# Kernel optimization log

Measured on AMD Instinct MI355X. Metric: run time of the kernel, lower is better.

## Reference

```python
import jax, jax.numpy as jnp
import numpy as np
from math import sqrt

D_LLM = 768
N_HEADS = 8
D_KEYS = 128


def setup_inputs() -> dict:
    key = jax.random.key(0)
    ks = jax.random.split(key, 9)
    B, T, N, S = 8, 96, 16, 1000
    dkh = D_KEYS * N_HEADS
    inp = {
        "time_series": jax.random.normal(ks[0], (B, T, N), dtype=jnp.float32),
        "source_embedding": jax.random.normal(ks[1], (S, D_LLM), dtype=jnp.float32),
        "value_embedding": jax.random.normal(ks[2], (S, D_LLM), dtype=jnp.float32),
        # key_projection: Linear(d_llm, d_keys*n_heads)
        "Wk": jax.random.normal(ks[3], (D_LLM, dkh), dtype=jnp.float32) / np.float32(sqrt(D_LLM)),
        "bk": jnp.zeros((dkh,), dtype=jnp.float32),
        # value_projection: Linear(d_llm, d_keys*n_heads)
        "Wv": jax.random.normal(ks[4], (D_LLM, dkh), dtype=jnp.float32) / np.float32(sqrt(D_LLM)),
        "bv": jnp.zeros((dkh,), dtype=jnp.float32),
        # out_projection: Linear(d_keys*n_heads, d_llm)
        "Wo": jax.random.normal(ks[5], (dkh, D_LLM), dtype=jnp.float32) / np.float32(sqrt(dkh)),
        "bo": jnp.zeros((D_LLM,), dtype=jnp.float32),
    }
    return inp


def reference(time_series, source_embedding, value_embedding, Wk, bk, Wv, bv, Wo, bo):
    B, T, N = time_series.shape
    S = source_embedding.shape[0]
    H, dk = N_HEADS, D_KEYS

    # (B,T,N) -> (B*N, T); Q repeats each scalar across d_keys*n_heads then nan->0
    ts = jnp.transpose(time_series, (0, 2, 1)).reshape(B * N, T)
    ts = jnp.where(jnp.isnan(ts), jnp.float32(0.0), ts)
    Q = jnp.broadcast_to(ts[:, :, None, None], (B * N, T, H, dk))  # bthe

    K = (source_embedding @ Wk + bk).reshape(S, H, dk)  # she
    V = (value_embedding @ Wv + bv).reshape(S, H, dk)   # she

    scale = jnp.float32(1.0 / sqrt(dk))
    scores = jnp.einsum('bthe,she->bhts', Q, K)          # [B*N, H, T, S]
    A = jax.nn.softmax(scale * scores, axis=-1)          # dropout = identity (eval)
    out = jnp.einsum('bhts,she->bthe', A, V).reshape(B * N, T, H * dk)
    return out @ Wo + bo                                 # [B*N, T, d_llm]
```

## Files before the change

kernel.cpp:

```cpp
#include <hip/hip_runtime.h>
#include <hip/hip_bf16.h>
#include <math.h>

#define D_LLM 768
#define DKH   1024
#define NH    8
#define DK    128
#define S_LEN 1000
#define S_PAD 1024
#define M_ROWS 12288
#define T_LEN 96
#define N_VARS 16

static constexpr float SCALE_EXP2 = (float)(0.08838834764831845 * 1.4426950408889634);

typedef __attribute__((ext_vector_type(8))) _Float16 half8;
typedef __attribute__((ext_vector_type(2))) _Float16 half2v;
typedef __attribute__((ext_vector_type(4))) float f32x4;

__device__ __forceinline__ half2v pkrtz(float a, float b) {
    return __builtin_bit_cast(half2v, __builtin_amdgcn_cvt_pkrtz(a, b));
}

__device__ __forceinline__ void gload_lds16(const void* g, void* l) {
    __builtin_amdgcn_global_load_lds(
        (const __attribute__((address_space(1))) unsigned int*)g,
        (__attribute__((address_space(3))) unsigned int*)l, 16, 0, 0);
}

__global__ __launch_bounds__(256) void prep_kernel(const float* __restrict__ vemb,
                                                   const float* __restrict__ Wv,
                                                   const float* __restrict__ Wo,
                                                   const float* __restrict__ Wk,
                                                   const float* __restrict__ bk,
                                                   _Float16* __restrict__ Ab16,
                                                   _Float16* __restrict__ Wvt,
                                                   _Float16* __restrict__ Wot,
                                                   float* __restrict__ Wksum,
                                                   float* __restrict__ bksum) {
    __shared__ float tl[32][33];
    int blk = blockIdx.x, tid = threadIdx.x;
    if (blk < 768) {
        int i4 = (blk * 256 + tid) * 4;
        float4 v = make_float4(0.f, 0.f, 0.f, 0.f);
        if (i4 < S_LEN * D_LLM) v = *(const float4*)(vemb + i4);
        short4 o;
        o.x = __builtin_bit_cast(short, (_Float16)v.x);
        o.y = __builtin_bit_cast(short, (_Float16)v.y);
        o.z = __builtin_bit_cast(short, (_Float16)v.z);
        o.w = __builtin_bit_cast(short, (_Float16)v.w);
        *(short4*)(Ab16 + i4) = o;
    } else if (blk < 1536) {
        int tau = blk - 768;
        int k0 = (tau % 24) * 32, n0 = (tau / 24) * 32;
        int tx = tid & 31, ty = tid >> 5;
        #pragma unroll
        for (int p = 0; p < 4; ++p)
            tl[ty + p * 8][tx] = Wv[(size_t)(k0 + ty + p * 8) * DKH + n0 + tx];
        __syncthreads();
        #pragma unroll
        for (int p = 0; p < 4; ++p)
            Wvt[(size_t)(n0 + ty + p * 8) * D_LLM + k0 + tx] = (_Float16)tl[tx][ty + p * 8];
    } else if (blk < 2304) {
        int tau = blk - 1536;
        int k0 = (tau & 31) * 32, n0 = (tau >> 5) * 32;
        int tx = tid & 31, ty = tid >> 5;
        #pragma unroll
        for (int p = 0; p < 4; ++p)
            tl[ty + p * 8][tx] = Wo[(size_t)(k0 + ty + p * 8) * D_LLM + n0 + tx];
        __syncthreads();
        #pragma unroll
        for (int p = 0; p < 4; ++p)
            Wot[(size_t)(n0 + ty + p * 8) * DKH + k0 + tx] = (_Float16)tl[tx][ty + p * 8];
    } else {
        int blk2 = blk - 2304;
        int w = tid >> 6, lane = tid & 63;
        if (blk2 < 192) {
            int d = blk2 * 4 + w;
            const float* p = Wk + (size_t)d * DKH + lane * 16;
            float s = 0.f;
            #pragma unroll
            for (int i = 0; i < 4; ++i) {
                float4 v = *(const float4*)(p + i * 4);
                s += v.x + v.y + v.z + v.w;
            }
            s += __shfl_down(s, 4);
            s += __shfl_down(s, 2);
            s += __shfl_down(s, 1);
            if ((lane & 7) == 0) Wksum[d * NH + (lane >> 3)] = s;
        } else if (w == 0) {
            const float* p = bk + lane * 16;
            float s = 0.f;
            #pragma unroll
            for (int i = 0; i < 4; ++i) {
                float4 v = *(const float4*)(p + i * 4);
                s += v.x + v.y + v.z + v.w;
            }
            s += __shfl_down(s, 4);
            s += __shfl_down(s, 2);
            s += __shfl_down(s, 1);
            if ((lane & 7) == 0) bksum[lane >> 3] = s;
        }
    }
}

__global__ __launch_bounds__(256) void kv_kernel(const float* __restrict__ src,
                                                 const float* __restrict__ Wksum,
                                                 const float* __restrict__ bksum,
                                                 float* __restrict__ Kpad,
                                                 const _Float16* __restrict__ A,
                                                 const _Float16* __restrict__ Bt,
                                                 const float* __restrict__ bias,
                                                 _Float16* __restrict__ Vt) {
    __shared__ _Float16 VAs[2][2048];
    __shared__ _Float16 VBs[2][2048];
    int tid = threadIdx.x;
    if (blockIdx.x < 256) {
        int w = tid >> 6, lane = tid & 63;
        int s = blockIdx.x * 4 + w;
        if (s >= S_LEN) {
            if (lane < 8) Kpad[lane * S_PAD + s] = 0.f;
            return;
        }
        const float* sp = src + (size_t)s * D_LLM + lane * 12;
        float xv[12];
        ((float4*)xv)[0] = *(const float4*)(sp);
        ((float4*)xv)[1] = *(const float4*)(sp + 4);
        ((float4*)xv)[2] = *(const float4*)(sp + 8);
        float a[8] = {0.f, 0.f, 0.f, 0.f, 0.f, 0.f, 0.f, 0.f};
        const float* wp = Wksum + lane * 12 * NH;
        #pragma unroll
        for (int i = 0; i < 12; ++i) {
            float4 wa = *(const float4*)(wp + i * 8);
            float4 wb = *(const float4*)(wp + i * 8 + 4);
            a[0] = fmaf(xv[i], wa.x, a[0]); a[1] = fmaf(xv[i], wa.y, a[1]);
            a[2] = fmaf(xv[i], wa.z, a[2]); a[3] = fmaf(xv[i], wa.w, a[3]);
            a[4] = fmaf(xv[i], wb.x, a[4]); a[5] = fmaf(xv[i], wb.y, a[5]);
            a[6] = fmaf(xv[i], wb.z, a[6]); a[7] = fmaf(xv[i], wb.w, a[7]);
        }
        #pragma unroll
        for (int off = 32; off > 0; off >>= 1) {
            #pragma unroll
            for (int hh = 0; hh < 8; ++hh) a[hh] += __shfl_xor(a[hh], off);
        }
        #pragma unroll
        for (int hh = 0; hh < 8; ++hh)
            if (lane == hh) Kpad[hh * S_PAD + s] = (a[hh] + bksum[hh]) * SCALE_EXP2;
        return;
    }
    int b2 = blockIdx.x - 256;
    int w = tid >> 6, lane = tid & 63;
    int bm0 = (b2 >> 4) * 64, bn0 = (b2 & 15) * 64;
    int lrow = tid >> 2, lcol = (tid & 3) * 8;
    const _Float16* ga = A + (size_t)(bm0 + lrow) * D_LLM + lcol;
    const _Float16* gb = Bt + (size_t)(bn0 + lrow) * D_LLM + lcol;

    f32x4 acc[2][2];
    #pragma unroll
    for (int m = 0; m < 2; ++m)
        #pragma unroll
        for (int n = 0; n < 2; ++n) acc[m][n] = (f32x4){0.f, 0.f, 0.f, 0.f};
    int sgrp = (lane >> 4) << 3;
    int arow = (w >> 1) * 32 + (lane & 15);
    int brow = (w & 1) * 32 + (lane & 15);

#define VSTAGE(buf, k0) do { \
        gload_lds16(ga + (k0), (char*)&VAs[buf][0] + w * 1024); \
        gload_lds16(gb + (k0), (char*)&VBs[buf][0] + w * 1024); } while (0)

    VSTAGE(0, 0);
    __syncthreads();
    #pragma unroll 2
    for (int tt = 0; tt < 24; ++tt) {
        int cur = tt & 1;
        if (tt < 23) VSTAGE(cur ^ 1, (tt + 1) * 32);
        const _Float16* Ac = &VAs[cur][0];
        const _Float16* Bc = &VBs[cur][0];
        half8 af[2], bf[2];
        #pragma unroll
        for (int m = 0; m < 2; ++m) af[m] = *(const half8*)(Ac + (arow + m * 16) * 32 + sgrp);
        #pragma unroll
        for (int n = 0; n < 2; ++n) bf[n] = *(const half8*)(Bc + (brow + n * 16) * 32 + sgrp);
        __builtin_amdgcn_s_setprio(1);
        #pragma unroll
        for (int m = 0; m < 2; ++m)
            #pragma unroll
            for (int n = 0; n < 2; ++n)
                acc[m][n] = __builtin_amdgcn_mfma_f32_16x16x32_f16(af[m], bf[n], acc[m][n], 0, 0, 0);
        __builtin_amdgcn_s_setprio(0);
        __syncthreads();
    }
#undef VSTAGE

    int rowoff = (lane >> 4) << 2;
    #pragma unroll
    for (int m = 0; m < 2; ++m) {
        #pragma unroll
        for (int n = 0; n < 2; ++n) {
            int c = bn0 + (w & 1) * 32 + n * 16 + (lane & 15);
            float b = bias[c];
            #pragma unroll
            for (int q = 0; q < 4; ++q) {
                int srow = bm0 + (w >> 1) * 32 + m * 16 + rowoff + q;
                float val = (srow < S_LEN) ? acc[m][n][q] + b : 0.f;
                Vt[(size_t)c * S_PAD + srow] = (_Float16)val;
            }
        }
    }
}

__device__ __forceinline__ void compute_afr(const float* kq, float x0, float x1,
                                            float nm0, float nm1, half8& o0, half8& o1) {
    float4 a = *(const float4*)kq;
    float4 b = *(const float4*)(kq + 4);
    float kv[8] = {a.x, a.y, a.z, a.w, b.x, b.y, b.z, b.w};
    union { half8 v; half2v h[4]; } u0, u1;
    #pragma unroll
    for (int j = 0; j < 4; ++j) {
        float w00 = __builtin_amdgcn_exp2f(fmaf(x0, kv[2 * j], nm0));
        float w01 = __builtin_amdgcn_exp2f(fmaf(x0, kv[2 * j + 1], nm0));
        u0.h[j] = pkrtz(w00, w01);
        float w10 = __builtin_amdgcn_exp2f(fmaf(x1, kv[2 * j], nm1));
        float w11 = __builtin_amdgcn_exp2f(fmaf(x1, kv[2 * j + 1], nm1));
        u1.h[j] = pkrtz(w10, w11);
    }
    o0 = u0.v; o1 = u1.v;
}

__global__ __launch_bounds__(256) void attn_mfma_kernel(const float* __restrict__ ts,
                                                        const float* __restrict__ Kpad,
                                                        const _Float16* __restrict__ Vt,
                                                        _Float16* __restrict__ attB) {
    __shared__ _Float16 Vs[4][2048];
    __shared__ float Krow[1024];
    __shared__ float red[8];
    const int tid = threadIdx.x;
    const int lane = tid & 63, w = tid >> 6;
    const int h = blockIdx.y;
    const int eh = blockIdx.z;
    const int m0 = blockIdx.x * 128 + w * 32;
    const int l15 = lane & 15, q = lane >> 4;

    const int erow = w * 16 + (lane >> 2);
    const int perm = (lane & 3) ^ (erow & 3);
    const _Float16* gsrc = Vt + (size_t)(h * DK + eh * 64 + erow) * S_PAD + perm * 8;
    const float* kg = Kpad + h * S_PAD;

    gload_lds16(kg + w * 256 + lane * 4, (char*)Krow + w * 1024);
    gload_lds16(gsrc, (char*)&Vs[0][0] + w * 1024);
    gload_lds16(gsrc + 32, (char*)&Vs[1][0] + w * 1024);
    gload_lds16(gsrc + 64, (char*)&Vs[2][0] + w * 1024);

    float x0, x1;
    {
        int m = m0 + l15;
        int rr = m / T_LEN;
        float v = ts[((size_t)(rr >> 4) * T_LEN + (m % T_LEN)) * N_VARS + (rr & 15)];
        x0 = (v != v) ? 0.f : v;
        m = m0 + 16 + l15;
        rr = m / T_LEN;
        v = ts[((size_t)(rr >> 4) * T_LEN + (m % T_LEN)) * N_VARS + (rr & 15)];
        x1 = (v != v) ? 0.f : v;
    }

    asm volatile("s_waitcnt vmcnt(3)" ::: "memory");
    __builtin_amdgcn_sched_barrier(0);
    __builtin_amdgcn_s_barrier();

    float mn, mx;
    {
        float4 k4 = *(const float4*)&Krow[tid * 4];
        if (tid < 250) {
            mx = fmaxf(fmaxf(k4.x, k4.y), fmaxf(k4.z, k4.w));
            mn = fminf(fminf(k4.x, k4.y), fminf(k4.z, k4.w));
        } else { mx = -3e38f; mn = 3e38f; }
        #pragma unroll
        for (int off = 32; off > 0; off >>= 1) {
            mx = fmaxf(mx, __shfl_xor(mx, off));
            mn = fminf(mn, __shfl_xor(mn, off));
        }
        if (lane == 0) { red[w * 2] = mn; red[w * 2 + 1] = mx; }
        asm volatile("s_waitcnt lgkmcnt(0)" ::: "memory");
        __builtin_amdgcn_sched_barrier(0);
        __builtin_amdgcn_s_barrier();
        mn = fminf(fminf(red[0], red[2]), fminf(red[4], red[6]));
        mx = fmaxf(fmaxf(red[1], red[3]), fmaxf(red[5], red[7]));
    }

    float nm0 = -((x0 >= 0.f) ? x0 * mx : x0 * mn);
    float nm1 = -((x1 >= 0.f) ? x1 * mx : x1 * mn);
    float wpadf0, wpadf1;
    {
        half2v p0 = pkrtz(__builtin_amdgcn_exp2f(nm0), 0.f);
        half2v p1 = pkrtz(__builtin_amdgcn_exp2f(nm1), 0.f);
        wpadf0 = (float)p0[0];
        wpadf1 = (float)p1[0];
    }

    f32x4 acc0[4], acc1[4];
    #pragma unroll
    for (int e = 0; e < 4; ++e) {
        acc0[e] = (f32x4){0.f, 0.f, 0.f, 0.f};
        acc1[e] = (f32x4){0.f, 0.f, 0.f, 0.f};
    }
    f32x4 accd0 = (f32x4){0.f, 0.f, 0.f, 0.f};
    f32x4 accd1 = (f32x4){0.f, 0.f, 0.f, 0.f};
    half8 ones;
    #pragma unroll
    for (int j = 0; j < 8; ++j) ones[j] = (_Float16)1.0f;

    const float* kvp = Krow + q * 8;
    half8 afrA0, afrA1, afrB0, afrB1;
    compute_afr(kvp, x0, x1, nm0, nm1, afrA0, afrA1);

    const int vofs = l15 * 64 + (((q ^ (l15 & 3)) & 3) << 4);

    #pragma unroll
    for (int kt = 0; kt < 32; ++kt) {
        if (kt < 30)      asm volatile("s_waitcnt vmcnt(2)" ::: "memory");
        else if (kt == 30) asm volatile("s_waitcnt vmcnt(1)" ::: "memory");
        else               asm volatile("s_waitcnt vmcnt(0)" ::: "memory");
        __builtin_amdgcn_sched_barrier(0);
        __builtin_amdgcn_s_barrier();
        if (kt <= 28)
            gload_lds16(gsrc + (kt + 3) * 32, (char*)&Vs[(kt + 3) & 3][0] + w * 1024);
        const char* cb = (const char*)&Vs[kt & 3][0];
        if (kt < 31) compute_afr(kvp + (kt + 1) * 32, x0, x1, nm0, nm1, afrB0, afrB1);
        #pragma unroll
        for (int et = 0; et < 4; ++et) {
            half8 bfv = *(const half8*)(cb + et * 1024 + vofs);
            acc0[et] = __builtin_amdgcn_mfma_f32_16x16x32_f16(afrA0, bfv, acc0[et], 0, 0, 0);
            acc1[et] = __builtin_amdgcn_mfma_f32_16x16x32_f16(afrA1, bfv, acc1[et], 0, 0, 0);
        }
        accd0 = __builtin_amdgcn_mfma_f32_16x16x32_f16(afrA0, ones, accd0, 0, 0, 0);
        accd1 = __builtin_amdgcn_mfma_f32_16x16x32_f16(afrA1, ones, accd1, 0, 0, 0);
        afrA0 = afrB0; afrA1 = afrB1;
    }

    int rowoff = q << 2;
    #pragma unroll
    for (int r = 0; r < 2; ++r) {
        #pragma unroll
        for (int qq = 0; qq < 4; ++qq) {
            float wp = __shfl(r ? wpadf1 : wpadf0, rowoff + qq);
            float den = (r ? accd1[qq] : accd0[qq]) - 24.f * wp;
            float inv = 1.f / den;
            int mrow = m0 + r * 16 + rowoff + qq;
            _Float16* op = attB + (size_t)mrow * DKH + h * DK + eh * 64 + l15;
            #pragma unroll
            for (int et = 0; et < 4; ++et)
                op[et * 16] = (_Float16)((r ? acc1[et][qq] : acc0[et][qq]) * inv);
        }
    }
}

__global__ __launch_bounds__(256) void outproj_kernel(const _Float16* __restrict__ A,
                                                      const _Float16* __restrict__ Bt,
                                                      const float* __restrict__ bo,
                                                      float* __restrict__ C) {
    __shared__ _Float16 As[3][4096];
    __shared__ _Float16 Bs[3][3072];
    int wg = blockIdx.x;
    wg = (wg & 7) * 96 + (wg >> 3);
    int bx = wg & 7, by = wg >> 3;
    int t = threadIdx.x, w = t >> 6, lane = t & 63;
    int bm0 = by * 128, bn0 = bx * 96;
    int lrow = t >> 2, lcol = (t & 3) * 8;
    const _Float16* ga0 = A + (size_t)(bm0 + lrow) * DKH + lcol;
    const _Float16* ga1 = ga0 + (size_t)64 * DKH;
    const _Float16* gb0 = Bt + (size_t)(bn0 + lrow) * DKH + lcol;
    const _Float16* gb1 = gb0 + (size_t)64 * DKH;

    f32x4 acc[4][3];
    #pragma unroll
    for (int m = 0; m < 4; ++m)
        #pragma unroll
        for (int n = 0; n < 3; ++n) acc[m][n] = (f32x4){0.f, 0.f, 0.f, 0.f};

    int sgrp = (lane >> 4) << 3;
    int arow = (w >> 1) * 64 + (lane & 15);
    int brow = (w & 1) * 48 + (lane & 15);

#define OSTAGE(bi, k0) do { \
        gload_lds16(ga0 + (k0), (char*)&As[bi][0] + w * 1024); \
        gload_lds16(ga1 + (k0), (char*)&As[bi][0] + 4096 + w * 1024); \
        gload_lds16(gb0 + (k0), (char*)&Bs[bi][0] + w * 1024); \
        if (w < 2) gload_lds16(gb1 + (k0), (char*)&Bs[bi][0] + 4096 + w * 1024); } while (0)

    OSTAGE(0, 0);
    OSTAGE(1, 32);
    #pragma unroll
    for (int kt = 0; kt < 32; ++kt) {
        if (kt == 31)   asm volatile("s_waitcnt vmcnt(0)" ::: "memory");
        else if (w < 2) asm volatile("s_waitcnt vmcnt(4)" ::: "memory");
        else            asm volatile("s_waitcnt vmcnt(3)" ::: "memory");
        __builtin_amdgcn_sched_barrier(0);
        __builtin_amdgcn_s_barrier();
        if (kt < 30) OSTAGE((kt + 2) % 3, (kt + 2) * 32);
        const _Float16* Ac = &As[kt % 3][0];
        const _Float16* Bc = &Bs[kt % 3][0];
        half8 af[4], bf[3];
        #pragma unroll
        for (int m = 0; m < 4; ++m) af[m] = *(const half8*)(Ac + (arow + m * 16) * 32 + sgrp);
        #pragma unroll
        for (int n = 0; n < 3; ++n) bf[n] = *(const half8*)(Bc + (brow + n * 16) * 32 + sgrp);
        __builtin_amdgcn_s_setprio(1);
        #pragma unroll
        for (int m = 0; m < 4; ++m)
            #pragma unroll
            for (int n = 0; n < 3; ++n)
                acc[m][n] = __builtin_amdgcn_mfma_f32_16x16x32_f16(af[m], bf[n], acc[m][n], 0, 0, 0);
        __builtin_amdgcn_s_setprio(0);
    }
#undef OSTAGE

    int rowoff = (lane >> 4) << 2;
    #pragma unroll
    for (int m = 0; m < 4; ++m) {
        #pragma unroll
        for (int n = 0; n < 3; ++n) {
            int col = bn0 + (w & 1) * 48 + n * 16 + (lane & 15);
            float b = bo[col];
            #pragma unroll
            for (int q = 0; q < 4; ++q) {
                int row = bm0 + (w >> 1) * 64 + m * 16 + rowoff + q;
                C[(size_t)row * D_LLM + col] = acc[m][n][q] + b;
            }
        }
    }
}

extern "C" void kernel_launch(void* const* d_in, const int* in_sizes, int n_in,
                              void* d_out, int out_size, void* d_ws, size_t ws_size,
                              hipStream_t stream) {
    const float* ts   = (const float*)d_in[0];
    const float* src  = (const float*)d_in[1];
    const float* vemb = (const float*)d_in[2];
    const float* Wk   = (const float*)d_in[3];
    const float* bk   = (const float*)d_in[4];
    const float* Wv   = (const float*)d_in[5];
    const float* bv   = (const float*)d_in[6];
    const float* Wo   = (const float*)d_in[7];
    const float* bo   = (const float*)d_in[8];
    float* out = (float*)d_out;

    float* ws = (float*)d_ws;
    float* Kpad   = ws;
    float* Wksum  = ws + 8192;
    float* bksum  = ws + 14336;
    _Float16* Vt   = (_Float16*)(ws + 14592);
    _Float16* Wot  = (_Float16*)(ws + 540672);
    _Float16* attB = (_Float16*)(ws + 936960);
    _Float16* Ab16 = (_Float16*)(ws + 936960);
    _Float16* Wvt  = (_Float16*)(ws + 1330176);

    prep_kernel<<<2497, 256, 0, stream>>>(vemb, Wv, Wo, Wk, bk, Ab16, Wvt, Wot, Wksum, bksum);
    kv_kernel<<<512, 256, 0, stream>>>(src, Wksum, bksum, Kpad, Ab16, Wvt, bv, Vt);
    {
        dim3 g(96, NH, 2);
        attn_mfma_kernel<<<g, 256, 0, stream>>>(ts, Kpad, Vt, attB);
    }
    outproj_kernel<<<768, 256, 0, stream>>>(attB, Wot, bo, out);
}
```

Measured before the change: 98.79 us.

## Restructure attention kernel to single-wave blocks computing 64 rows by full head

Replaces the 4-wave, half-head-width attention blocks with single-wave blocks that each compute 64 query rows across all 128 value columns of a head. This removes the split over the value dimension, so the exp2 weight computation is no longer duplicated across two blocks, and drops block-level barriers in favour of per-wave waitcnt double buffering. In exchange each wave holds far more accumulators (4x8 MFMA tiles), raising register pressure and possibly lowering occupancy. The pipeline also shrinks from four buffers to two.

```diff
diff --git a/kernel.cpp b/kernel.cpp
--- a/kernel.cpp
+++ b/kernel.cpp
@@ -209,147 +209,137 @@
     }
 }
 
-__device__ __forceinline__ void compute_afr(const float* kq, float x0, float x1,
-                                            float nm0, float nm1, half8& o0, half8& o1) {
-    float4 a = *(const float4*)kq;
-    float4 b = *(const float4*)(kq + 4);
-    float kv[8] = {a.x, a.y, a.z, a.w, b.x, b.y, b.z, b.w};
-    union { half8 v; half2v h[4]; } u0, u1;
-    #pragma unroll
-    for (int j = 0; j < 4; ++j) {
-        float w00 = __builtin_amdgcn_exp2f(fmaf(x0, kv[2 * j], nm0));
-        float w01 = __builtin_amdgcn_exp2f(fmaf(x0, kv[2 * j + 1], nm0));
-        u0.h[j] = pkrtz(w00, w01);
-        float w10 = __builtin_amdgcn_exp2f(fmaf(x1, kv[2 * j], nm1));
-        float w11 = __builtin_amdgcn_exp2f(fmaf(x1, kv[2 * j + 1], nm1));
-        u1.h[j] = pkrtz(w10, w11);
-    }
-    o0 = u0.v; o1 = u1.v;
-}
-
-__global__ __launch_bounds__(256) void attn_mfma_kernel(const float* __restrict__ ts,
-                                                        const float* __restrict__ Kpad,
-                                                        const _Float16* __restrict__ Vt,
-                                                        _Float16* __restrict__ attB) {
-    __shared__ _Float16 Vs[4][2048];
+__global__ __launch_bounds__(64) void attn_mfma_kernel(const float* __restrict__ ts,
+                                                       const float* __restrict__ Kpad,
+                                                       const _Float16* __restrict__ Vt,
+                                                       _Float16* __restrict__ attB) {
+    __shared__ _Float16 Vs[2][4096];
     __shared__ float Krow[1024];
-    __shared__ float red[8];
-    const int tid = threadIdx.x;
-    const int lane = tid & 63, w = tid >> 6;
+    const int lane = threadIdx.x;
     const int h = blockIdx.y;
-    const int eh = blockIdx.z;
-    const int m0 = blockIdx.x * 128 + w * 32;
+    const int m0 = blockIdx.x * 64;
     const int l15 = lane & 15, q = lane >> 4;
-
-    const int erow = w * 16 + (lane >> 2);
-    const int perm = (lane & 3) ^ (erow & 3);
-    const _Float16* gsrc = Vt + (size_t)(h * DK + eh * 64 + erow) * S_PAD + perm * 8;
+    char* VsB = (char*)&Vs[0][0];
+
     const float* kg = Kpad + h * S_PAD;
-
-    gload_lds16(kg + w * 256 + lane * 4, (char*)Krow + w * 1024);
-    gload_lds16(gsrc, (char*)&Vs[0][0] + w * 1024);
-    gload_lds16(gsrc + 32, (char*)&Vs[1][0] + w * 1024);
-    gload_lds16(gsrc + 64, (char*)&Vs[2][0] + w * 1024);
-
-    float x0, x1;
-    {
-        int m = m0 + l15;
+    #pragma unroll
+    for (int j = 0; j < 4; ++j)
+        gload_lds16(kg + j * 256 + lane * 4, (char*)Krow + j * 1024);
+
+    const int seg = (lane & 3) ^ ((lane >> 2) & 3);
+    const _Float16* gsrc = Vt + (size_t)(h * DK + (lane >> 2)) * S_PAD + seg * 8;
+#define STAGE(ck) do { \
+        _Pragma("unroll") \
+        for (int j = 0; j < 8; ++j) \
+            gload_lds16(gsrc + (size_t)j * 16 * S_PAD + (ck) * 32, \
+                        VsB + ((ck) & 1) * 8192 + j * 1024); } while (0)
+    STAGE(0);
+    STAGE(1);
+
+    float x[4];
+    #pragma unroll
+    for (int r = 0; r < 4; ++r) {
+        int m = m0 + r * 16 + l15;
         int rr = m / T_LEN;
         float v = ts[((size_t)(rr >> 4) * T_LEN + (m % T_LEN)) * N_VARS + (rr & 15)];
-        x0 = (v != v) ? 0.f : v;
-        m = m0 + 16 + l15;
-        rr = m / T_LEN;
-        v = ts[((size_t)(rr >> 4) * T_LEN + (m % T_LEN)) * N_VARS + (rr & 15)];
-        x1 = (v != v) ? 0.f : v;
-    }
-
-    asm volatile("s_waitcnt vmcnt(3)" ::: "memory");
+        x[r] = (v != v) ? 0.f : v;
+    }
+
+    asm volatile("s_waitcnt vmcnt(16)" ::: "memory");
     __builtin_amdgcn_sched_barrier(0);
-    __builtin_amdgcn_s_barrier();
-
-    float mn, mx;
-    {
-        float4 k4 = *(const float4*)&Krow[tid * 4];
-        if (tid < 250) {
-            mx = fmaxf(fmaxf(k4.x, k4.y), fmaxf(k4.z, k4.w));
-            mn = fminf(fminf(k4.x, k4.y), fminf(k4.z, k4.w));
-        } else { mx = -3e38f; mn = 3e38f; }
-        #pragma unroll
-        for (int off = 32; off > 0; off >>= 1) {
-            mx = fmaxf(mx, __shfl_xor(mx, off));
-            mn = fminf(mn, __shfl_xor(mn, off));
-        }
-        if (lane == 0) { red[w * 2] = mn; red[w * 2 + 1] = mx; }
+
+    float mn = 3e38f, mx = -3e38f;
+    #pragma unroll
+    for (int j = 0; j < 4; ++j) {
+        float4 k4 = *(const float4*)&Krow[lane * 16 + j * 4];
+        mx = fmaxf(mx, fmaxf(fmaxf(k4.x, k4.y), fmaxf(k4.z, k4.w)));
+        mn = fminf(mn, fminf(fminf(k4.x, k4.y), fminf(k4.z, k4.w)));
+    }
+    #pragma unroll
+    for (int off = 32; off > 0; off >>= 1) {
+        mx = fmaxf(mx, __shfl_xor(mx, off));
+        mn = fminf(mn, __shfl_xor(mn, off));
+    }
+
+    float nm[4], wpadf[4];
+    #pragma unroll
+    for (int r = 0; r < 4; ++r) {
+        nm[r] = -((x[r] >= 0.f) ? x[r] * mx : x[r] * mn);
+        half2v p = pkrtz(__builtin_amdgcn_exp2f(nm[r]), 0.f);
+        wpadf[r] = (float)p[0];
+    }
+
+    f32x4 acc[4][8];
+    #pragma unroll
+    for (int r = 0; r < 4; ++r)
+        #pragma unroll
+        for (int e = 0; e < 8; ++e) acc[r][e] = (f32x4){0.f, 0.f, 0.f, 0.f};
+    f32x4 accd[4];
+    #pragma unroll
+    for (int r = 0; r < 4; ++r) accd[r] = (f32x4){0.f, 0.f, 0.f, 0.f};
+    half8 ones;
+    #pragma unroll
+    for (int j = 0; j < 8; ++j) ones[j] = (_Float16)1.0f;
+
+#define CHUNK(kt) do { \
+        const char* cb = VsB + ((kt) & 1) * 8192; \
+        const float* kvp = Krow + (kt) * 32 + q * 8; \
+        float4 ka = *(const float4*)kvp; \
+        float4 kb = *(const float4*)(kvp + 4); \
+        float kv[8] = {ka.x, ka.y, ka.z, ka.w, kb.x, kb.y, kb.z, kb.w}; \
+        half8 afr[4]; \
+        _Pragma("unroll") \
+        for (int r = 0; r < 4; ++r) { \
+            union { half8 v; half2v hh[4]; } u; \
+            _Pragma("unroll") \
+            for (int j = 0; j < 4; ++j) { \
+                float w0 = __builtin_amdgcn_exp2f(fmaf(x[r], kv[2 * j], nm[r])); \
+                float w1 = __builtin_amdgcn_exp2f(fmaf(x[r], kv[2 * j + 1], nm[r])); \
+                u.hh[j] = pkrtz(w0, w1); \
+            } \
+            afr[r] = u.v; \
+        } \
+        _Pragma("unroll") \
+        for (int et = 0; et < 8; ++et) { \
+            half8 bfv = *(const half8*)(cb + (et * 16 + l15) * 64 + ((q ^ (l15 & 3)) << 4)); \
+            _Pragma("unroll") \
+            for (int r = 0; r < 4; ++r) \
+                acc[r][et] = __builtin_amdgcn_mfma_f32_16x16x32_f16(afr[r], bfv, acc[r][et], 0, 0, 0); \
+        } \
+        _Pragma("unroll") \
+        for (int r = 0; r < 4; ++r) \
+            accd[r] = __builtin_amdgcn_mfma_f32_16x16x32_f16(afr[r], ones, accd[r], 0, 0, 0); } while (0)
+
+    for (int kt = 0; kt < 30; ++kt) {
+        asm volatile("s_waitcnt vmcnt(8)" ::: "memory");
+        __builtin_amdgcn_sched_barrier(0);
+        CHUNK(kt);
         asm volatile("s_waitcnt lgkmcnt(0)" ::: "memory");
         __builtin_amdgcn_sched_barrier(0);
-        __builtin_amdgcn_s_barrier();
-        mn = fminf(fminf(red[0], red[2]), fminf(red[4], red[6]));
-        mx = fmaxf(fmaxf(red[1], red[3]), fmaxf(red[5], red[7]));
-    }
-
-    float nm0 = -((x0 >= 0.f) ? x0 * mx : x0 * mn);
-    float nm1 = -((x1 >= 0.f) ? x1 * mx : x1 * mn);
-    float wpadf0, wpadf1;
-    {
-        half2v p0 = pkrtz(__builtin_amdgcn_exp2f(nm0), 0.f);
-        half2v p1 = pkrtz(__builtin_amdgcn_exp2f(nm1), 0.f);
-        wpadf0 = (float)p0[0];
-        wpadf1 = (float)p1[0];
-    }
-
-    f32x4 acc0[4], acc1[4];
-    #pragma unroll
-    for (int e = 0; e < 4; ++e) {
-        acc0[e] = (f32x4){0.f, 0.f, 0.f, 0.f};
-        acc1[e] = (f32x4){0.f, 0.f, 0.f, 0.f};
-    }
-    f32x4 accd0 = (f32x4){0.f, 0.f, 0.f, 0.f};
-    f32x4 accd1 = (f32x4){0.f, 0.f, 0.f, 0.f};
-    half8 ones;
-    #pragma unroll
-    for (int j = 0; j < 8; ++j) ones[j] = (_Float16)1.0f;
-
-    const float* kvp = Krow + q * 8;
-    half8 afrA0, afrA1, afrB0, afrB1;
-    compute_afr(kvp, x0, x1, nm0, nm1, afrA0, afrA1);
-
-    const int vofs = l15 * 64 + (((q ^ (l15 & 3)) & 3) << 4);
-
-    #pragma unroll
-    for (int kt = 0; kt < 32; ++kt) {
-        if (kt < 30)      asm volatile("s_waitcnt vmcnt(2)" ::: "memory");
-        else if (kt == 30) asm volatile("s_waitcnt vmcnt(1)" ::: "memory");
-        else               asm volatile("s_waitcnt vmcnt(0)" ::: "memory");
-        __builtin_amdgcn_sched_barrier(0);
-        __builtin_amdgcn_s_barrier();
-        if (kt <= 28)
-            gload_lds16(gsrc + (kt + 3) * 32, (char*)&Vs[(kt + 3) & 3][0] + w * 1024);
-        const char* cb = (const char*)&Vs[kt & 3][0];
-        if (kt < 31) compute_afr(kvp + (kt + 1) * 32, x0, x1, nm0, nm1, afrB0, afrB1);
-        #pragma unroll
-        for (int et = 0; et < 4; ++et) {
-            half8 bfv = *(const half8*)(cb + et * 1024 + vofs);
-            acc0[et] = __builtin_amdgcn_mfma_f32_16x16x32_f16(afrA0, bfv, acc0[et], 0, 0, 0);
-            acc1[et] = __builtin_amdgcn_mfma_f32_16x16x32_f16(afrA1, bfv, acc1[et], 0, 0, 0);
-        }
-        accd0 = __builtin_amdgcn_mfma_f32_16x16x32_f16(afrA0, ones, accd0, 0, 0, 0);
-        accd1 = __builtin_amdgcn_mfma_f32_16x16x32_f16(afrA1, ones, accd1, 0, 0, 0);
-        afrA0 = afrB0; afrA1 = afrB1;
-    }
+        STAGE(kt + 2);
+    }
+    asm volatile("s_waitcnt vmcnt(8)" ::: "memory");
+    __builtin_amdgcn_sched_barrier(0);
+    CHUNK(30);
+    asm volatile("s_waitcnt vmcnt(0)" ::: "memory");
+    __builtin_amdgcn_sched_barrier(0);
+    CHUNK(31);
+#undef CHUNK
+#undef STAGE
 
     int rowoff = q << 2;
     #pragma unroll
-    for (int r = 0; r < 2; ++r) {
+    for (int r = 0; r < 4; ++r) {
         #pragma unroll
         for (int qq = 0; qq < 4; ++qq) {
-            float wp = __shfl(r ? wpadf1 : wpadf0, rowoff + qq);
-            float den = (r ? accd1[qq] : accd0[qq]) - 24.f * wp;
+            float wp = __shfl(wpadf[r], rowoff + qq);
+            float den = accd[r][qq] - 24.f * wp;
             float inv = 1.f / den;
             int mrow = m0 + r * 16 + rowoff + qq;
-            _Float16* op = attB + (size_t)mrow * DKH + h * DK + eh * 64 + l15;
-            #pragma unroll
-            for (int et = 0; et < 4; ++et)
-                op[et * 16] = (_Float16)((r ? acc1[et][qq] : acc0[et][qq]) * inv);
+            _Float16* op = attB + (size_t)mrow * DKH + h * DK + l15;
+            #pragma unroll
+            for (int et = 0; et < 8; ++et)
+                op[et * 16] = (_Float16)(acc[r][et][qq] * inv);
         }
     }
 }
@@ -457,8 +447,8 @@
     prep_kernel<<<2497, 256, 0, stream>>>(vemb, Wv, Wo, Wk, bk, Ab16, Wvt, Wot, Wksum, bksum);
     kv_kernel<<<512, 256, 0, stream>>>(src, Wksum, bksum, Kpad, Ab16, Wvt, bv, Vt);
     {
-        dim3 g(96, NH, 2);
-        attn_mfma_kernel<<<g, 256, 0, stream>>>(ts, Kpad, Vt, attB);
+        dim3 g(192, NH);
+        attn_mfma_kernel<<<g, 64, 0, stream>>>(ts, Kpad, Vt, attB);
     }
     outproj_kernel<<<768, 256, 0, stream>>>(attB, Wot, bo, out);
 }
```

Result: slower. 116.2 us (+17.6%).
